# Performance work log

Hardware: AMD Instinct MI355X
Metric: run time of the kernel (lower is better)

## Reference

```python
import jax, jax.numpy as jnp
import numpy as np

N = 262144   # number of occupied voxels (sparse points)
CH = 96      # channels
K = 27       # 3x3x3 kernel offsets


def setup_inputs() -> dict:
    key = jax.random.key(0)
    ks = jax.random.split(key, 6)
    feats = jax.random.normal(ks[0], (N, CH), jnp.float32)
    neighbor_idx = jax.random.randint(ks[1], (K, N), 0, N, jnp.int32)
    mask = jax.random.randint(ks[2], (K, N), 0, 2, jnp.int32).astype(bool)
    center = K // 2  # center offset is always the point itself
    neighbor_idx = neighbor_idx.at[center].set(jnp.arange(N, dtype=jnp.int32))
    mask = mask.at[center].set(True)
    scale = np.float32(1.0 / np.sqrt(K * CH))
    W1 = jax.random.normal(ks[3], (K, CH, CH), jnp.float32) * scale
    W2 = jax.random.normal(ks[4], (K, CH, CH), jnp.float32) * scale
    b1 = jnp.zeros((CH,), jnp.float32)
    b2 = jnp.zeros((CH,), jnp.float32)
    a1 = jnp.full((1,), 0.25, jnp.float32)  # MinkowskiPReLU default
    a2 = jnp.full((1,), 0.25, jnp.float32)
    return dict(feats=feats, neighbor_idx=neighbor_idx, mask=mask,
                W1=W1, b1=b1, a1=a1, W2=W2, b2=b2, a2=a2)


def _sparse_conv(f, idx, m, W, b):
    # gather-GEMM-scatter over K kernel offsets; scan keeps memory at one
    # gathered [N, CH] slab at a time instead of [K, N, CH].
    def body(acc, kmaps):
        ik, mk, Wk = kmaps
        g = jnp.where(mk[:, None], f[ik], jnp.zeros((), f.dtype))  # gather [N, CH]
        return acc + g @ Wk, None
    acc0 = jnp.zeros((f.shape[0], W.shape[-1]), f.dtype)
    out, _ = jax.lax.scan(body, acc0, (idx, m, W))
    return out + b


def _prelu(x, a):
    return jnp.where(x > 0, x, a * x)


def reference(feats, neighbor_idx, mask, W1, b1, a1, W2, b2, a2):
    x = _prelu(_sparse_conv(feats, neighbor_idx, mask, W1, b1), a1)
    x = _sparse_conv(x, neighbor_idx, mask, W2, b2)
    return _prelu(x + feats, a2)  # in-place residual add then PReLU
```

## Files before the change

kernel.cpp:

```cpp
#include <hip/hip_runtime.h>
#include <hip/hip_bf16.h>

#define CH     96
#define KOFF   27
#define TM     256
#define NCHUNK 1152

typedef __bf16 bf16x8 __attribute__((ext_vector_type(8)));
typedef float  floatx4 __attribute__((ext_vector_type(4)));

typedef const __attribute__((address_space(1))) unsigned int* as1_u32p;
typedef __attribute__((address_space(3))) unsigned int*       as3_u32p;

static __device__ inline uint pk_bf16(float a, float b) {
    __hip_bfloat162 h = __float22bfloat162_rn(make_float2(a, b));
    return *(uint*)&h;
}

static __device__ inline void frag_block(int k, const float* __restrict__ W1,
                                         const float* __restrict__ W2,
                                         uint4* __restrict__ Wf1,
                                         uint4* __restrict__ Wf2)
{
    const float* src = (k < KOFF) ? (W1 + (size_t)k * CH * CH)
                                  : (W2 + (size_t)(k - KOFF) * CH * CH);
    uint4* dst = ((k < KOFF) ? Wf1 : Wf2) + (size_t)(k % KOFF) * NCHUNK;
    for (int c = threadIdx.x; c < 1152; c += 256) {
        int f    = c >> 6;
        int lane = c & 63;
        int nt = f / 3, kk = f - nt * 3;
        int jb  = kk * 32 + (lane >> 4) * 8;
        int col = nt * 16 + (lane & 15);
        uint p[4];
#pragma unroll
        for (int h = 0; h < 4; ++h)
            p[h] = pk_bf16(src[(size_t)(jb + 2 * h) * CH + col],
                           src[(size_t)(jb + 2 * h + 1) * CH + col]);
        uint4 v; v.x = p[0]; v.y = p[1]; v.z = p[2]; v.w = p[3];
        dst[c] = v;
    }
}

__global__ __launch_bounds__(256) void prep_all(
    const float* __restrict__ W1, const float* __restrict__ W2,
    uint4* __restrict__ Wf1, uint4* __restrict__ Wf2,
    const float* __restrict__ feats, const int* __restrict__ nmask,
    uint4* __restrict__ xb, uint* __restrict__ pb, int N)
{
    const int bid = blockIdx.x;
    if (bid < 2 * KOFF) { frag_block(bid, W1, W2, Wf1, Wf2); return; }

    const int tid    = (bid - 2 * KOFF) * 256 + threadIdx.x;
    const int stride = (gridDim.x - 2 * KOFF) * 256;
    const int nv = N * (CH / 8);
    const float4* fs = (const float4*)feats;
    for (int i = tid; i < nv; i += stride) {
        float4 lo = fs[(size_t)2 * i], hi = fs[(size_t)2 * i + 1];
        uint4 v;
        v.x = pk_bf16(lo.x, lo.y); v.y = pk_bf16(lo.z, lo.w);
        v.z = pk_bf16(hi.x, hi.y); v.w = pk_bf16(hi.z, hi.w);
        xb[i] = v;
    }
    for (int i = tid; i < N; i += stride) {
        uint m = 0;
        for (int k = 0; k < KOFF; ++k)
            m |= (nmask[(size_t)k * N + i] != 0 ? 1u : 0u) << k;
        pb[i] = m;
    }
}

__global__ __launch_bounds__(256) void make_frags(
    const float* __restrict__ W1, const float* __restrict__ W2,
    uint4* __restrict__ Wf1, uint4* __restrict__ Wf2)
{
    frag_block(blockIdx.x, W1, W2, Wf1, Wf2);
}

template<int PASS>
__global__ __launch_bounds__(512, 5) void sconv(
    const void* __restrict__ fin_,
    const int*  __restrict__ nidx,
    const int*  __restrict__ nmask,
    const uint* __restrict__ pb,
    const uint4* __restrict__ Wf,
    const float* __restrict__ bias,
    const float* __restrict__ alpha,
    const float* __restrict__ resid,
    void* __restrict__ fout_,
    int N)
{
    __shared__ uint4 WsL[2 * NCHUNK];

    const int tid   = threadIdx.x;
    const int lane  = tid & 63;
    const int wid   = tid >> 6;
    const int quad  = lane >> 4;
    const int col0  = lane & 15;
    const int wbase = blockIdx.x * TM + wid * 32;
    const int myrow = wbase + (lane & 31);

    uint mbits;
    if (pb) {
        mbits = pb[myrow];
    } else {
        mbits = 0;
        for (int k = 0; k < KOFF; ++k)
            mbits |= (nmask[(size_t)k * N + myrow] != 0 ? 1u : 0u) << k;
    }
    const uint mb0 = (uint)__shfl((int)mbits, col0, 64);
    const uint mb1 = (uint)__shfl((int)mbits, 16 + col0, 64);

    {
        const uint4* g = Wf;
#pragma unroll
        for (int r = 0; r < 2; ++r) {
            int cbase = r * 512 + wid * 64;
            __builtin_amdgcn_global_load_lds(
                (as1_u32p)(const void*)(g + cbase + lane),
                (as3_u32p)(void*)(&WsL[cbase]), 16, 0, 0);
        }
        if (wid < 2) {
            int cbase = 1024 + wid * 64;
            __builtin_amdgcn_global_load_lds(
                (as1_u32p)(const void*)(g + cbase + lane),
                (as3_u32p)(void*)(&WsL[cbase]), 16, 0, 0);
        }
    }

    int idxv = nidx[myrow];

    floatx4 acc[2][6];
#pragma unroll
    for (int mt = 0; mt < 2; ++mt)
#pragma unroll
        for (int nt = 0; nt < 6; ++nt)
            acc[mt][nt] = (floatx4){0.f, 0.f, 0.f, 0.f};

    for (int k = 0; k < KOFF; ++k) {
        const int buf = k & 1;
        const int i0  = __shfl(idxv, col0, 64);
        const int i1  = __shfl(idxv, 16 + col0, 64);
        const bool s0 = (mb0 >> k) & 1u;
        const bool s1 = (mb1 >> k) & 1u;

        __syncthreads();

        if (k + 1 < KOFF) {
            const uint4* g = Wf + (size_t)(k + 1) * NCHUNK;
            const int dst = (buf ^ 1) * NCHUNK;
#pragma unroll
            for (int r = 0; r < 2; ++r) {
                int cbase = r * 512 + wid * 64;
                __builtin_amdgcn_global_load_lds(
                    (as1_u32p)(const void*)(g + cbase + lane),
                    (as3_u32p)(void*)(&WsL[dst + cbase]), 16, 0, 0);
            }
            if (wid < 2) {
                int cbase = 1024 + wid * 64;
                __builtin_amdgcn_global_load_lds(
                    (as1_u32p)(const void*)(g + cbase + lane),
                    (as3_u32p)(void*)(&WsL[dst + cbase]), 16, 0, 0);
            }
            idxv = nidx[(size_t)(k + 1) * N + myrow];
        }

#pragma unroll
        for (int kk = 0; kk < 3; ++kk) {
            uint4 r0 = {0, 0, 0, 0}, r1 = {0, 0, 0, 0};
            if (PASS == 2) {
                const float4* fs = (const float4*)fin_;
                if (s0) {
                    float4 lo = fs[(size_t)i0 * 24 + kk * 8 + quad * 2];
                    float4 hi = fs[(size_t)i0 * 24 + kk * 8 + quad * 2 + 1];
                    r0.x = pk_bf16(lo.x, lo.y); r0.y = pk_bf16(lo.z, lo.w);
                    r0.z = pk_bf16(hi.x, hi.y); r0.w = pk_bf16(hi.z, hi.w);
                }
                if (s1) {
                    float4 lo = fs[(size_t)i1 * 24 + kk * 8 + quad * 2];
                    float4 hi = fs[(size_t)i1 * 24 + kk * 8 + quad * 2 + 1];
                    r1.x = pk_bf16(lo.x, lo.y); r1.y = pk_bf16(lo.z, lo.w);
                    r1.z = pk_bf16(hi.x, hi.y); r1.w = pk_bf16(hi.z, hi.w);
                }
            } else {
                const uint4* xs = (const uint4*)fin_;
                if (s0) r0 = xs[(size_t)i0 * 12 + kk * 4 + quad];
                if (s1) r1 = xs[(size_t)i1 * 12 + kk * 4 + quad];
            }
            bf16x8 a0 = *(bf16x8*)&r0;
            bf16x8 a1 = *(bf16x8*)&r1;
#pragma unroll
            for (int nt = 0; nt < 6; ++nt) {
                bf16x8 b = *(bf16x8*)&WsL[buf * NCHUNK + (nt * 3 + kk) * 64 + lane];
                acc[0][nt] = __builtin_amdgcn_mfma_f32_16x16x32_bf16(a0, b, acc[0][nt], 0, 0, 0);
                acc[1][nt] = __builtin_amdgcn_mfma_f32_16x16x32_bf16(a1, b, acc[1][nt], 0, 0, 0);
            }
        }
    }

    const float al = alpha[0];
#pragma unroll
    for (int mt = 0; mt < 2; ++mt) {
#pragma unroll
        for (int nt = 0; nt < 6; ++nt) {
            const int c  = nt * 16 + col0;
            const float bv = bias[c];
#pragma unroll
            for (int rr = 0; rr < 4; ++rr) {
                const int row = wbase + mt * 16 + quad * 4 + rr;
                float v = acc[mt][nt][rr] + bv;
                if (PASS == 1) v += resid[(size_t)row * CH + c];
                v = (v > 0.f) ? v : al * v;
                if (PASS == 1) {
                    ((float*)fout_)[(size_t)row * CH + c] = v;
                } else {
                    __hip_bfloat16 h = __float2bfloat16(v);
                    ((ushort*)fout_)[(size_t)row * CH + c] = *(ushort*)&h;
                }
            }
        }
    }
}

extern "C" void kernel_launch(void* const* d_in, const int* in_sizes, int n_in,
                              void* d_out, int out_size, void* d_ws, size_t ws_size,
                              hipStream_t stream)
{
    const float* feats = (const float*)d_in[0];
    const int*   nidx  = (const int*)d_in[1];
    const int*   nmask = (const int*)d_in[2];
    const float* W1    = (const float*)d_in[3];
    const float* b1    = (const float*)d_in[4];
    const float* a1    = (const float*)d_in[5];
    const float* W2    = (const float*)d_in[6];
    const float* b2    = (const float*)d_in[7];
    const float* a2    = (const float*)d_in[8];

    const int N = in_sizes[0] / CH;

    uint4*  Wf1 = (uint4*)d_ws;
    uint4*  Wf2 = Wf1 + (size_t)KOFF * NCHUNK;
    ushort* x   = (ushort*)(Wf2 + (size_t)KOFF * NCHUNK);
    ushort* xb  = x + (size_t)N * CH;
    uint*   pb  = (uint*)(xb + (size_t)N * CH);
    const size_t need_full = (size_t)((char*)(pb + N) - (char*)d_ws);
    const bool full = ws_size >= need_full;

    if (full) {
        prep_all<<<2 * KOFF + 2048, 256, 0, stream>>>(
            W1, W2, Wf1, Wf2, feats, nmask, (uint4*)xb, pb, N);
        sconv<0><<<N / TM, 512, 0, stream>>>(
            (const void*)xb, nidx, nullptr, pb, Wf1, b1, a1, nullptr, (void*)x, N);
        sconv<1><<<N / TM, 512, 0, stream>>>(
            (const void*)x, nidx, nullptr, pb, Wf2, b2, a2, feats, d_out, N);
    } else {
        make_frags<<<2 * KOFF, 256, 0, stream>>>(W1, W2, Wf1, Wf2);
        sconv<2><<<N / TM, 512, 0, stream>>>(
            (const void*)feats, nidx, nmask, nullptr, Wf1, b1, a1, nullptr, (void*)x, N);
        sconv<1><<<N / TM, 512, 0, stream>>>(
            (const void*)x, nidx, nmask, nullptr, Wf2, b2, a2, feats, d_out, N);
    }
}
```

Before: 542.0 us.

## Software-pipeline neighbor gathers in bf16 pass and vectorize mask packing

In the bf16-input conv pass, the gathered neighbor rows for offset k+1 are now loaded into registers while the MFMAs for offset k run, which is meant to hide gather latency behind compute. To fit the extra registers, the launch bound drops from 5 to 4 waves per SIMD, which lowers occupancy. The mask bit-packing in the prep kernel now reads int4 vectors and writes four packed masks per thread, cutting the number of memory transactions. The float-input pass is unchanged.

```diff
diff --git a/kernel.cpp b/kernel.cpp
--- a/kernel.cpp
+++ b/kernel.cpp
@@ -61,11 +61,20 @@
         v.z = pk_bf16(hi.x, hi.y); v.w = pk_bf16(hi.z, hi.w);
         xb[i] = v;
     }
-    for (int i = tid; i < N; i += stride) {
-        uint m = 0;
-        for (int k = 0; k < KOFF; ++k)
-            m |= (nmask[(size_t)k * N + i] != 0 ? 1u : 0u) << k;
-        pb[i] = m;
+    const int4* nm4 = (const int4*)nmask;
+    const int n4 = N / 4;
+    for (int i = tid; i < n4; i += stride) {
+        uint m0 = 0, m1 = 0, m2 = 0, m3 = 0;
+#pragma unroll
+        for (int k = 0; k < KOFF; ++k) {
+            int4 v = nm4[(size_t)k * n4 + i];
+            m0 |= (v.x != 0 ? 1u : 0u) << k;
+            m1 |= (v.y != 0 ? 1u : 0u) << k;
+            m2 |= (v.z != 0 ? 1u : 0u) << k;
+            m3 |= (v.w != 0 ? 1u : 0u) << k;
+        }
+        uint4 o; o.x = m0; o.y = m1; o.z = m2; o.w = m3;
+        ((uint4*)pb)[i] = o;
     }
 }
 
@@ -77,7 +86,7 @@
 }
 
 template<int PASS>
-__global__ __launch_bounds__(512, 5) void sconv(
+__global__ __launch_bounds__(512, 4) void sconv(
     const void* __restrict__ fin_,
     const int*  __restrict__ nidx,
     const int*  __restrict__ nmask,
@@ -127,8 +136,6 @@
         }
     }
 
-    int idxv = nidx[myrow];
-
     floatx4 acc[2][6];
 #pragma unroll
     for (int mt = 0; mt < 2; ++mt)
@@ -136,38 +143,39 @@
         for (int nt = 0; nt < 6; ++nt)
             acc[mt][nt] = (floatx4){0.f, 0.f, 0.f, 0.f};
 
-    for (int k = 0; k < KOFF; ++k) {
-        const int buf = k & 1;
-        const int i0  = __shfl(idxv, col0, 64);
-        const int i1  = __shfl(idxv, 16 + col0, 64);
-        const bool s0 = (mb0 >> k) & 1u;
-        const bool s1 = (mb1 >> k) & 1u;
-
-        __syncthreads();
-
-        if (k + 1 < KOFF) {
-            const uint4* g = Wf + (size_t)(k + 1) * NCHUNK;
-            const int dst = (buf ^ 1) * NCHUNK;
-#pragma unroll
-            for (int r = 0; r < 2; ++r) {
-                int cbase = r * 512 + wid * 64;
-                __builtin_amdgcn_global_load_lds(
-                    (as1_u32p)(const void*)(g + cbase + lane),
-                    (as3_u32p)(void*)(&WsL[dst + cbase]), 16, 0, 0);
-            }
-            if (wid < 2) {
-                int cbase = 1024 + wid * 64;
-                __builtin_amdgcn_global_load_lds(
-                    (as1_u32p)(const void*)(g + cbase + lane),
-                    (as3_u32p)(void*)(&WsL[dst + cbase]), 16, 0, 0);
-            }
-            idxv = nidx[(size_t)(k + 1) * N + myrow];
-        }
-
-#pragma unroll
-        for (int kk = 0; kk < 3; ++kk) {
-            uint4 r0 = {0, 0, 0, 0}, r1 = {0, 0, 0, 0};
-            if (PASS == 2) {
+    if (PASS == 2) {
+        int idxv = nidx[myrow];
+        for (int k = 0; k < KOFF; ++k) {
+            const int buf = k & 1;
+            const int i0  = __shfl(idxv, col0, 64);
+            const int i1  = __shfl(idxv, 16 + col0, 64);
+            const bool s0 = (mb0 >> k) & 1u;
+            const bool s1 = (mb1 >> k) & 1u;
+
+            __syncthreads();
+
+            if (k + 1 < KOFF) {
+                const uint4* g = Wf + (size_t)(k + 1) * NCHUNK;
+                const int dst = (buf ^ 1) * NCHUNK;
+#pragma unroll
+                for (int r = 0; r < 2; ++r) {
+                    int cbase = r * 512 + wid * 64;
+                    __builtin_amdgcn_global_load_lds(
+                        (as1_u32p)(const void*)(g + cbase + lane),
+                        (as3_u32p)(void*)(&WsL[dst + cbase]), 16, 0, 0);
+                }
+                if (wid < 2) {
+                    int cbase = 1024 + wid * 64;
+                    __builtin_amdgcn_global_load_lds(
+                        (as1_u32p)(const void*)(g + cbase + lane),
+                        (as3_u32p)(void*)(&WsL[dst + cbase]), 16, 0, 0);
+                }
+                idxv = nidx[(size_t)(k + 1) * N + myrow];
+            }
+
+#pragma unroll
+            for (int kk = 0; kk < 3; ++kk) {
+                uint4 r0 = {0, 0, 0, 0}, r1 = {0, 0, 0, 0};
                 const float4* fs = (const float4*)fin_;
                 if (s0) {
                     float4 lo = fs[(size_t)i0 * 24 + kk * 8 + quad * 2];
@@ -181,18 +189,89 @@
                     r1.x = pk_bf16(lo.x, lo.y); r1.y = pk_bf16(lo.z, lo.w);
                     r1.z = pk_bf16(hi.x, hi.y); r1.w = pk_bf16(hi.z, hi.w);
                 }
-            } else {
-                const uint4* xs = (const uint4*)fin_;
-                if (s0) r0 = xs[(size_t)i0 * 12 + kk * 4 + quad];
-                if (s1) r1 = xs[(size_t)i1 * 12 + kk * 4 + quad];
-            }
-            bf16x8 a0 = *(bf16x8*)&r0;
-            bf16x8 a1 = *(bf16x8*)&r1;
-#pragma unroll
-            for (int nt = 0; nt < 6; ++nt) {
-                bf16x8 b = *(bf16x8*)&WsL[buf * NCHUNK + (nt * 3 + kk) * 64 + lane];
-                acc[0][nt] = __builtin_amdgcn_mfma_f32_16x16x32_bf16(a0, b, acc[0][nt], 0, 0, 0);
-                acc[1][nt] = __builtin_amdgcn_mfma_f32_16x16x32_bf16(a1, b, acc[1][nt], 0, 0, 0);
+                bf16x8 a0 = *(bf16x8*)&r0;
+                bf16x8 a1 = *(bf16x8*)&r1;
+#pragma unroll
+                for (int nt = 0; nt < 6; ++nt) {
+                    bf16x8 b = *(bf16x8*)&WsL[buf * NCHUNK + (nt * 3 + kk) * 64 + lane];
+                    acc[0][nt] = __builtin_amdgcn_mfma_f32_16x16x32_bf16(a0, b, acc[0][nt], 0, 0, 0);
+                    acc[1][nt] = __builtin_amdgcn_mfma_f32_16x16x32_bf16(a1, b, acc[1][nt], 0, 0, 0);
+                }
+            }
+        }
+    } else {
+        const uint4* xs = (const uint4*)fin_;
+        int idx_cur = nidx[myrow];
+        uint4 gc0[3], gc1[3];
+        {
+            const int i0 = __shfl(idx_cur, col0, 64);
+            const int i1 = __shfl(idx_cur, 16 + col0, 64);
+            const bool s0 = mb0 & 1u;
+            const bool s1 = mb1 & 1u;
+#pragma unroll
+            for (int kk = 0; kk < 3; ++kk) {
+                gc0[kk] = (uint4){0, 0, 0, 0};
+                gc1[kk] = (uint4){0, 0, 0, 0};
+                if (s0) gc0[kk] = xs[(size_t)i0 * 12 + kk * 4 + quad];
+                if (s1) gc1[kk] = xs[(size_t)i1 * 12 + kk * 4 + quad];
+            }
+        }
+        int idx_nxt = nidx[(size_t)N + myrow];
+
+        for (int k = 0; k < KOFF; ++k) {
+            const int buf = k & 1;
+
+            __syncthreads();
+
+            uint4 gn0[3], gn1[3];
+            if (k + 1 < KOFF) {
+                const uint4* g = Wf + (size_t)(k + 1) * NCHUNK;
+                const int dst = (buf ^ 1) * NCHUNK;
+#pragma unroll
+                for (int r = 0; r < 2; ++r) {
+                    int cbase = r * 512 + wid * 64;
+                    __builtin_amdgcn_global_load_lds(
+                        (as1_u32p)(const void*)(g + cbase + lane),
+                        (as3_u32p)(void*)(&WsL[dst + cbase]), 16, 0, 0);
+                }
+                if (wid < 2) {
+                    int cbase = 1024 + wid * 64;
+                    __builtin_amdgcn_global_load_lds(
+                        (as1_u32p)(const void*)(g + cbase + lane),
+                        (as3_u32p)(void*)(&WsL[dst + cbase]), 16, 0, 0);
+                }
+                const int i0n = __shfl(idx_nxt, col0, 64);
+                const int i1n = __shfl(idx_nxt, 16 + col0, 64);
+                const bool t0 = (mb0 >> (k + 1)) & 1u;
+                const bool t1 = (mb1 >> (k + 1)) & 1u;
+#pragma unroll
+                for (int kk = 0; kk < 3; ++kk) {
+                    gn0[kk] = (uint4){0, 0, 0, 0};
+                    gn1[kk] = (uint4){0, 0, 0, 0};
+                    if (t0) gn0[kk] = xs[(size_t)i0n * 12 + kk * 4 + quad];
+                    if (t1) gn1[kk] = xs[(size_t)i1n * 12 + kk * 4 + quad];
+                }
+                if (k + 2 < KOFF) idx_nxt = nidx[(size_t)(k + 2) * N + myrow];
+            }
+
+#pragma unroll
+            for (int kk = 0; kk < 3; ++kk) {
+                bf16x8 a0 = *(bf16x8*)&gc0[kk];
+                bf16x8 a1 = *(bf16x8*)&gc1[kk];
+#pragma unroll
+                for (int nt = 0; nt < 6; ++nt) {
+                    bf16x8 b = *(bf16x8*)&WsL[buf * NCHUNK + (nt * 3 + kk) * 64 + lane];
+                    acc[0][nt] = __builtin_amdgcn_mfma_f32_16x16x32_bf16(a0, b, acc[0][nt], 0, 0, 0);
+                    acc[1][nt] = __builtin_amdgcn_mfma_f32_16x16x32_bf16(a1, b, acc[1][nt], 0, 0, 0);
+                }
+            }
+
+            if (k + 1 < KOFF) {
+#pragma unroll
+                for (int kk = 0; kk < 3; ++kk) {
+                    gc0[kk] = gn0[kk];
+                    gc1[kk] = gn1[kk];
+                }
             }
         }
     }
```

Result: faster. 524.7 us, median of 2 (-3.2%).
